# Optimization experiments

Measured on AMD Instinct MI355X. Metric: run time of the kernel, lower is better.

Reference implementation:

```python
import jax, jax.numpy as jnp
import numpy as np

N_HEAD = 12

def setup_inputs() -> dict:
    key = jax.random.key(0)
    ks = jax.random.split(key, 5)
    B, T, C = 2, 2048, 768
    s = 0.02
    return {
        "x": jax.random.normal(ks[0], (B, T, C), jnp.float32),
        "c_attn_w": jax.random.normal(ks[1], (C, 3 * C), jnp.float32) * s,
        "c_attn_b": jax.random.normal(ks[2], (3 * C,), jnp.float32) * s,
        "c_proj_w": jax.random.normal(ks[3], (C, C), jnp.float32) * s,
        "c_proj_b": jax.random.normal(ks[4], (C,), jnp.float32) * s,
    }

def reference(x, c_attn_w, c_attn_b, c_proj_w, c_proj_b):
    B, T, C = x.shape
    H = N_HEAD
    D = C // H
    qkv = x @ c_attn_w + c_attn_b              # [B,T,3C]
    q, k, v = jnp.split(qkv, 3, axis=-1)
    # [B,T,C] -> [B,H,T,D]
    q = q.reshape(B, T, H, D).transpose(0, 2, 1, 3)
    k = k.reshape(B, T, H, D).transpose(0, 2, 1, 3)
    v = v.reshape(B, T, H, D).transpose(0, 2, 1, 3)
    att = jnp.einsum('bhqd,bhkd->bhqk', q, k) * (1.0 / np.sqrt(D))
    causal = jnp.tril(jnp.ones((T, T), bool))  # [T,T]
    att = jnp.where(causal[None, None], att, jnp.float32(-jnp.inf))
    att = jax.nn.softmax(att, axis=-1)
    y = jnp.einsum('bhqk,bhkd->bhqd', att, v)  # [B,H,T,D]
    y = y.transpose(0, 2, 1, 3).reshape(B, T, C)
    return y @ c_proj_w + c_proj_b
```

## Files before the change

kernel.cpp:

```cpp
#include <hip/hip_runtime.h>
#include <hip/hip_bf16.h>


using half4   = __attribute__((ext_vector_type(4))) _Float16;
using half8   = __attribute__((ext_vector_type(8))) _Float16;
using floatx4 = __attribute__((ext_vector_type(4))) float;

#define T_SEQ 2048
#define NHEAD 12
#define HDIM 64
#define C3 2304
#define CDIM 768
#define BT 4096

static __device__ inline _Float16 f2h(float f) { return (_Float16)f; }

__global__ __launch_bounds__(256)
void prologue(const float* __restrict__ x, const float* __restrict__ wa,
              const float* __restrict__ wp, _Float16* __restrict__ xb,
              _Float16* __restrict__ wTa, _Float16* __restrict__ wTp) {
    __shared__ float tile[32][33];
    int blk = blockIdx.x, tid = threadIdx.x;
    if (blk < 2304) {
        const float* w; _Float16* wT; int K, N, bx, by;
        if (blk < 1728) { w = wa; wT = wTa; K = CDIM; N = C3; bx = blk % 72; by = blk / 72; }
        else { int b2 = blk - 1728; w = wp; wT = wTp; K = CDIM; N = CDIM; bx = b2 % 24; by = b2 / 24; }
        int tx = tid & 31, ty = tid >> 5;
        #pragma unroll
        for (int j = 0; j < 32; j += 8) {
            int k = by * 32 + ty + j, n = bx * 32 + tx;
            tile[ty + j][tx] = w[(long)k * N + n];
        }
        __syncthreads();
        #pragma unroll
        for (int j = 0; j < 32; j += 8) {
            int nO = bx * 32 + ty + j, kO = by * 32 + tx;
            wT[(long)nO * K + kO] = f2h(tile[tx][ty + j]);
        }
    } else {
        int b2 = blk - 2304;
        long base = (long)b2 * 1536;
        #pragma unroll
        for (int j = 0; j < 6; ++j) {
            long i = base + j * 256 + tid;
            xb[i] = f2h(x[i]);
        }
    }
}

__global__ __launch_bounds__(256)
void gemm_qkv(const _Float16* __restrict__ A, const _Float16* __restrict__ Bt,
              const float* __restrict__ bias,
              _Float16* __restrict__ Qb, _Float16* __restrict__ Kb,
              _Float16* __restrict__ Vt) {
    __shared__ __align__(16) _Float16 As[128 * 32];
    __shared__ __align__(16) _Float16 Bs[64 * 32];
    const int K = CDIM;
    int tid = threadIdx.x;
    int m0 = blockIdx.x * 128, n0 = blockIdx.y * 64;
    int w = tid >> 6, l = tid & 63;
    int wm = (w >> 1) * 64, wn = (w & 1) * 32;
    int lr = l & 15, lq = l >> 4;

    int ea0 = tid * 8, ea1 = (256 + tid) * 8;
    int ra0 = ea0 >> 5, ca0 = ea0 & 31, ra1 = ea1 >> 5, ca1 = ea1 & 31;
    int eb = tid * 8, rb = eb >> 5, cb = eb & 31;

    floatx4 acc[4][2] = {};

    half8 Ar0 = *(const half8*)&A[(long)(m0 + ra0) * K + ca0];
    half8 Ar1 = *(const half8*)&A[(long)(m0 + ra1) * K + ca1];
    half8 Br  = *(const half8*)&Bt[(long)(n0 + rb) * K + cb];

    for (int kb = 0; kb < K; kb += 32) {
        *(half8*)&As[ea0] = Ar0;
        *(half8*)&As[ea1] = Ar1;
        *(half8*)&Bs[eb]  = Br;
        __syncthreads();
        if (kb + 32 < K) {
            Ar0 = *(const half8*)&A[(long)(m0 + ra0) * K + kb + 32 + ca0];
            Ar1 = *(const half8*)&A[(long)(m0 + ra1) * K + kb + 32 + ca1];
            Br  = *(const half8*)&Bt[(long)(n0 + rb) * K + kb + 32 + cb];
        }
        half8 af[4], bf[2];
        #pragma unroll
        for (int i = 0; i < 4; ++i)
            af[i] = *(const half8*)&As[(wm + i * 16 + lr) * 32 + lq * 8];
        #pragma unroll
        for (int i = 0; i < 2; ++i)
            bf[i] = *(const half8*)&Bs[(wn + i * 16 + lr) * 32 + lq * 8];
        #pragma unroll
        for (int mi = 0; mi < 4; ++mi)
            #pragma unroll
            for (int ni = 0; ni < 2; ++ni)
                acc[mi][ni] = __builtin_amdgcn_mfma_f32_16x16x32_f16(af[mi], bf[ni], acc[mi][ni], 0, 0, 0);
        __syncthreads();
    }

    int region = n0 / CDIM;
    if (region < 2) {
        _Float16* O = region ? Kb : Qb;
        int nc0 = n0 - region * CDIM + wn;
        #pragma unroll
        for (int mi = 0; mi < 4; ++mi)
            #pragma unroll
            for (int ni = 0; ni < 2; ++ni) {
                int col = nc0 + ni * 16 + lr;
                float bsc = bias[region * CDIM + col];
                #pragma unroll
                for (int r = 0; r < 4; ++r) {
                    int row = m0 + wm + mi * 16 + lq * 4 + r;
                    O[(long)row * CDIM + col] = f2h(acc[mi][ni][r] + bsc);
                }
            }
    } else {
        #pragma unroll
        for (int mi = 0; mi < 4; ++mi)
            #pragma unroll
            for (int ni = 0; ni < 2; ++ni) {
                int cv = n0 - 2 * CDIM + wn + ni * 16 + lr;
                float bsc = bias[2 * CDIM + cv];
                int h = cv >> 6, d = cv & 63;
                int t0 = m0 + wm + mi * 16 + lq * 4;
                int bb = t0 >> 11, t = t0 & 2047;
                half4 hv;
                #pragma unroll
                for (int r = 0; r < 4; ++r) hv[r] = f2h(acc[mi][ni][r] + bsc);
                *(half4*)&Vt[(((long)bb * NHEAD + h) * HDIM + d) * T_SEQ + t] = hv;
            }
    }
}

__global__ __launch_bounds__(256)
void gemm_proj(const _Float16* __restrict__ A, const _Float16* __restrict__ Bt,
               const float* __restrict__ bias, float* __restrict__ Cout,
               int M, int N, int K) {
    __shared__ __align__(16) _Float16 As[64 * 32];
    __shared__ __align__(16) _Float16 Bs[64 * 32];
    int tid = threadIdx.x;
    int m0 = blockIdx.x * 64, n0 = blockIdx.y * 64;
    int w = tid >> 6, l = tid & 63;
    int wm = (w >> 1) * 32, wn = (w & 1) * 32;
    int lr = l & 15, lq = l >> 4;

    int e = tid * 8, re = e >> 5, ce = e & 31;

    floatx4 acc[2][2] = {};

    half8 Ar = *(const half8*)&A[(long)(m0 + re) * K + ce];
    half8 Br = *(const half8*)&Bt[(long)(n0 + re) * K + ce];

    for (int kb = 0; kb < K; kb += 32) {
        *(half8*)&As[e] = Ar;
        *(half8*)&Bs[e] = Br;
        __syncthreads();
        if (kb + 32 < K) {
            Ar = *(const half8*)&A[(long)(m0 + re) * K + kb + 32 + ce];
            Br = *(const half8*)&Bt[(long)(n0 + re) * K + kb + 32 + ce];
        }
        half8 af[2], bf[2];
        #pragma unroll
        for (int i = 0; i < 2; ++i) {
            af[i] = *(const half8*)&As[(wm + i * 16 + lr) * 32 + lq * 8];
            bf[i] = *(const half8*)&Bs[(wn + i * 16 + lr) * 32 + lq * 8];
        }
        #pragma unroll
        for (int mi = 0; mi < 2; ++mi)
            #pragma unroll
            for (int ni = 0; ni < 2; ++ni)
                acc[mi][ni] = __builtin_amdgcn_mfma_f32_16x16x32_f16(af[mi], bf[ni], acc[mi][ni], 0, 0, 0);
        __syncthreads();
    }
    #pragma unroll
    for (int mi = 0; mi < 2; ++mi)
        #pragma unroll
        for (int ni = 0; ni < 2; ++ni) {
            int col = n0 + wn + ni * 16 + lr;
            float b = bias[col];
            #pragma unroll
            for (int r = 0; r < 4; ++r) {
                int row = m0 + wm + mi * 16 + lq * 4 + r;
                Cout[(long)row * N + col] = acc[mi][ni][r] + b;
            }
        }
}

__global__ __launch_bounds__(256)
void attn_kernel(const _Float16* __restrict__ Qb, const _Float16* __restrict__ Kb,
                 const _Float16* __restrict__ Vt, _Float16* __restrict__ y) {
    __shared__ __align__(16) _Float16 Ks[64 * 72];
    __shared__ __align__(16) _Float16 Vs[64 * 72];
    __shared__ __align__(16) _Float16 Ps[4][16 * 72];
    int tid = threadIdx.x;
    int w = tid >> 6, l = tid & 63;
    int lr = l & 15, lq = l >> 4;
    int blk = blockIdx.x;
    int bh = blk % (2 * NHEAD);
    int qb = 31 - blk / (2 * NHEAD);
    int b = bh / NHEAD, h = bh % NHEAD;
    int q0 = qb * 64 + w * 16;

    const _Float16* Qp = Qb + (long)b * T_SEQ * CDIM + h * HDIM;
    const _Float16* Kg = Kb + (long)b * T_SEQ * CDIM + h * HDIM;
    const _Float16* Vg = Vt + (long)bh * HDIM * T_SEQ;

    int r0 = tid >> 3, c0 = (tid & 7) * 8;
    int r1 = r0 + 32;

    const float qscale = 0.125f * 1.44269504f;
    half8 aq[2];
    #pragma unroll
    for (int kk = 0; kk < 2; ++kk) {
        aq[kk] = *(const half8*)&Qp[(long)(q0 + lr) * CDIM + kk * 32 + lq * 8];
        #pragma unroll
        for (int j = 0; j < 8; ++j) aq[kk][j] = f2h((float)aq[kk][j] * qscale);
    }

    half8 Kr0 = *(const half8*)&Kg[(long)r0 * CDIM + c0];
    half8 Kr1 = *(const half8*)&Kg[(long)r1 * CDIM + c0];
    half8 Vr0 = *(const half8*)&Vg[(long)r0 * T_SEQ + c0];
    half8 Vr1 = *(const half8*)&Vg[(long)r1 * T_SEQ + c0];

    float psum[4] = {0.f, 0.f, 0.f, 0.f};
    floatx4 acc[4] = {};

    for (int kt = 0; kt <= qb; ++kt) {
        int kbase = kt * 64;
        *(half8*)&Ks[r0 * 72 + c0] = Kr0;
        *(half8*)&Ks[r1 * 72 + c0] = Kr1;
        *(half8*)&Vs[r0 * 72 + c0] = Vr0;
        *(half8*)&Vs[r1 * 72 + c0] = Vr1;
        __syncthreads();
        if (kt < qb) {
            int nb = kbase + 64;
            Kr0 = *(const half8*)&Kg[(long)(nb + r0) * CDIM + c0];
            Kr1 = *(const half8*)&Kg[(long)(nb + r1) * CDIM + c0];
            Vr0 = *(const half8*)&Vg[(long)r0 * T_SEQ + nb + c0];
            Vr1 = *(const half8*)&Vg[(long)r1 * T_SEQ + nb + c0];
        }

        floatx4 sacc[4] = {};
        #pragma unroll
        for (int s = 0; s < 4; ++s)
            #pragma unroll
            for (int kk = 0; kk < 2; ++kk) {
                half8 bk = *(const half8*)&Ks[(s * 16 + lr) * 72 + kk * 32 + lq * 8];
                sacc[s] = __builtin_amdgcn_mfma_f32_16x16x32_f16(aq[kk], bk, sacc[s], 0, 0, 0);
            }

        if (kt == qb) {
            #pragma unroll
            for (int r = 0; r < 4; ++r) {
                int row = q0 + lq * 4 + r;
                #pragma unroll
                for (int s = 0; s < 4; ++s) {
                    float p = (kbase + s * 16 + lr > row) ? 0.f
                              : __builtin_amdgcn_exp2f(sacc[s][r]);
                    psum[r] += p;
                    Ps[w][(lq * 4 + r) * 72 + s * 16 + lr] = f2h(p);
                }
            }
        } else {
            #pragma unroll
            for (int r = 0; r < 4; ++r) {
                #pragma unroll
                for (int s = 0; s < 4; ++s) {
                    float p = __builtin_amdgcn_exp2f(sacc[s][r]);
                    psum[r] += p;
                    Ps[w][(lq * 4 + r) * 72 + s * 16 + lr] = f2h(p);
                }
            }
        }

        half8 ap0 = *(const half8*)&Ps[w][lr * 72 + lq * 8];
        half8 ap1 = *(const half8*)&Ps[w][lr * 72 + 32 + lq * 8];
        #pragma unroll
        for (int n = 0; n < 4; ++n) {
            #pragma unroll
            for (int kk = 0; kk < 2; ++kk) {
                half8 bv = *(const half8*)&Vs[(n * 16 + lr) * 72 + kk * 32 + lq * 8];
                acc[n] = __builtin_amdgcn_mfma_f32_16x16x32_f16(kk ? ap1 : ap0, bv, acc[n], 0, 0, 0);
            }
        }
        __syncthreads();
    }

    float l_i[4];
    #pragma unroll
    for (int r = 0; r < 4; ++r) {
        float s = psum[r];
        #pragma unroll
        for (int off = 1; off < 16; off <<= 1)
            s += __shfl_xor(s, off, 64);
        l_i[r] = s;
    }

    #pragma unroll
    for (int n = 0; n < 4; ++n)
        #pragma unroll
        for (int r = 0; r < 4; ++r) {
            int row = q0 + lq * 4 + r;
            float v = acc[n][r] / l_i[r];
            y[((long)(b * T_SEQ) + row) * CDIM + h * HDIM + n * 16 + lr] = f2h(v);
        }
}

extern "C" void kernel_launch(void* const* d_in, const int* in_sizes, int n_in,
                              void* d_out, int out_size, void* d_ws, size_t ws_size,
                              hipStream_t stream) {
    const float* x      = (const float*)d_in[0];
    const float* w_attn = (const float*)d_in[1];
    const float* b_attn = (const float*)d_in[2];
    const float* w_proj = (const float*)d_in[3];
    const float* b_proj = (const float*)d_in[4];
    float* out = (float*)d_out;

    char* ws = (char*)d_ws;
    _Float16* xb  = (_Float16*)(ws);
    _Float16* wTa = (_Float16*)(ws + 6291456);
    _Float16* wTp = (_Float16*)(ws + 9830400);
    _Float16* Qb  = (_Float16*)(ws + 11010048);
    _Float16* Kb  = (_Float16*)(ws + 17301504);
    _Float16* Vt  = (_Float16*)(ws + 23592960);
    _Float16* yb  = (_Float16*)(ws + 29884416);

    prologue<<<4352, 256, 0, stream>>>(x, w_attn, w_proj, xb, wTa, wTp);

    gemm_qkv<<<dim3(BT / 128, C3 / 64), 256, 0, stream>>>(xb, wTa, b_attn, Qb, Kb, Vt);

    attn_kernel<<<2 * NHEAD * (T_SEQ / 64), 256, 0, stream>>>(Qb, Kb, Vt, yb);

    gemm_proj<<<dim3(BT / 64, CDIM / 64), 256, 0, stream>>>(yb, wTp, b_proj, out, BT, CDIM, CDIM);
}
```

Measured before the change: 157.7 us.

## Split attention over key chunks and merge partials in projection GEMM

The causal attention kernel now splits each query tile's key range into two halves, handled by separate blocks. This doubles the grid and is meant to even out the load imbalance caused by causal masking. Each block writes unnormalised fp32 partial outputs and row sums to workspace. The output projection GEMM now loads both partials, adds them, normalises with a reciprocal and converts to fp16 while staging its A tile. The QKV and projection GEMMs also widen their N tile to 128. The price is extra fp32 global traffic for the partials, larger per-block register and LDS use, and fewer GEMM blocks.

```diff
diff --git a/kernel.cpp b/kernel.cpp
--- a/kernel.cpp
+++ b/kernel.cpp
@@ -12,6 +12,7 @@
 #define C3 2304
 #define CDIM 768
 #define BT 4096
+#define BH 24
 
 static __device__ inline _Float16 f2h(float f) { return (_Float16)f; }
 
@@ -54,45 +55,46 @@
               _Float16* __restrict__ Qb, _Float16* __restrict__ Kb,
               _Float16* __restrict__ Vt) {
     __shared__ __align__(16) _Float16 As[128 * 32];
-    __shared__ __align__(16) _Float16 Bs[64 * 32];
+    __shared__ __align__(16) _Float16 Bs[128 * 32];
     const int K = CDIM;
     int tid = threadIdx.x;
-    int m0 = blockIdx.x * 128, n0 = blockIdx.y * 64;
+    int m0 = blockIdx.x * 128, n0 = blockIdx.y * 128;
     int w = tid >> 6, l = tid & 63;
-    int wm = (w >> 1) * 64, wn = (w & 1) * 32;
+    int wm = (w >> 1) * 64, wn = (w & 1) * 64;
     int lr = l & 15, lq = l >> 4;
 
     int ea0 = tid * 8, ea1 = (256 + tid) * 8;
     int ra0 = ea0 >> 5, ca0 = ea0 & 31, ra1 = ea1 >> 5, ca1 = ea1 & 31;
-    int eb = tid * 8, rb = eb >> 5, cb = eb & 31;
-
-    floatx4 acc[4][2] = {};
+
+    floatx4 acc[4][4] = {};
 
     half8 Ar0 = *(const half8*)&A[(long)(m0 + ra0) * K + ca0];
     half8 Ar1 = *(const half8*)&A[(long)(m0 + ra1) * K + ca1];
-    half8 Br  = *(const half8*)&Bt[(long)(n0 + rb) * K + cb];
+    half8 Br0 = *(const half8*)&Bt[(long)(n0 + ra0) * K + ca0];
+    half8 Br1 = *(const half8*)&Bt[(long)(n0 + ra1) * K + ca1];
 
     for (int kb = 0; kb < K; kb += 32) {
         *(half8*)&As[ea0] = Ar0;
         *(half8*)&As[ea1] = Ar1;
-        *(half8*)&Bs[eb]  = Br;
+        *(half8*)&Bs[ea0] = Br0;
+        *(half8*)&Bs[ea1] = Br1;
         __syncthreads();
         if (kb + 32 < K) {
             Ar0 = *(const half8*)&A[(long)(m0 + ra0) * K + kb + 32 + ca0];
             Ar1 = *(const half8*)&A[(long)(m0 + ra1) * K + kb + 32 + ca1];
-            Br  = *(const half8*)&Bt[(long)(n0 + rb) * K + kb + 32 + cb];
-        }
-        half8 af[4], bf[2];
-        #pragma unroll
-        for (int i = 0; i < 4; ++i)
+            Br0 = *(const half8*)&Bt[(long)(n0 + ra0) * K + kb + 32 + ca0];
+            Br1 = *(const half8*)&Bt[(long)(n0 + ra1) * K + kb + 32 + ca1];
+        }
+        half8 af[4], bf[4];
+        #pragma unroll
+        for (int i = 0; i < 4; ++i) {
             af[i] = *(const half8*)&As[(wm + i * 16 + lr) * 32 + lq * 8];
-        #pragma unroll
-        for (int i = 0; i < 2; ++i)
             bf[i] = *(const half8*)&Bs[(wn + i * 16 + lr) * 32 + lq * 8];
+        }
         #pragma unroll
         for (int mi = 0; mi < 4; ++mi)
             #pragma unroll
-            for (int ni = 0; ni < 2; ++ni)
+            for (int ni = 0; ni < 4; ++ni)
                 acc[mi][ni] = __builtin_amdgcn_mfma_f32_16x16x32_f16(af[mi], bf[ni], acc[mi][ni], 0, 0, 0);
         __syncthreads();
     }
@@ -104,7 +106,7 @@
         #pragma unroll
         for (int mi = 0; mi < 4; ++mi)
             #pragma unroll
-            for (int ni = 0; ni < 2; ++ni) {
+            for (int ni = 0; ni < 4; ++ni) {
                 int col = nc0 + ni * 16 + lr;
                 float bsc = bias[region * CDIM + col];
                 #pragma unroll
@@ -117,7 +119,7 @@
         #pragma unroll
         for (int mi = 0; mi < 4; ++mi)
             #pragma unroll
-            for (int ni = 0; ni < 2; ++ni) {
+            for (int ni = 0; ni < 4; ++ni) {
                 int cv = n0 - 2 * CDIM + wn + ni * 16 + lr;
                 float bsc = bias[2 * CDIM + cv];
                 int h = cv >> 6, d = cv & 63;
@@ -132,62 +134,9 @@
 }
 
 __global__ __launch_bounds__(256)
-void gemm_proj(const _Float16* __restrict__ A, const _Float16* __restrict__ Bt,
-               const float* __restrict__ bias, float* __restrict__ Cout,
-               int M, int N, int K) {
-    __shared__ __align__(16) _Float16 As[64 * 32];
-    __shared__ __align__(16) _Float16 Bs[64 * 32];
-    int tid = threadIdx.x;
-    int m0 = blockIdx.x * 64, n0 = blockIdx.y * 64;
-    int w = tid >> 6, l = tid & 63;
-    int wm = (w >> 1) * 32, wn = (w & 1) * 32;
-    int lr = l & 15, lq = l >> 4;
-
-    int e = tid * 8, re = e >> 5, ce = e & 31;
-
-    floatx4 acc[2][2] = {};
-
-    half8 Ar = *(const half8*)&A[(long)(m0 + re) * K + ce];
-    half8 Br = *(const half8*)&Bt[(long)(n0 + re) * K + ce];
-
-    for (int kb = 0; kb < K; kb += 32) {
-        *(half8*)&As[e] = Ar;
-        *(half8*)&Bs[e] = Br;
-        __syncthreads();
-        if (kb + 32 < K) {
-            Ar = *(const half8*)&A[(long)(m0 + re) * K + kb + 32 + ce];
-            Br = *(const half8*)&Bt[(long)(n0 + re) * K + kb + 32 + ce];
-        }
-        half8 af[2], bf[2];
-        #pragma unroll
-        for (int i = 0; i < 2; ++i) {
-            af[i] = *(const half8*)&As[(wm + i * 16 + lr) * 32 + lq * 8];
-            bf[i] = *(const half8*)&Bs[(wn + i * 16 + lr) * 32 + lq * 8];
-        }
-        #pragma unroll
-        for (int mi = 0; mi < 2; ++mi)
-            #pragma unroll
-            for (int ni = 0; ni < 2; ++ni)
-                acc[mi][ni] = __builtin_amdgcn_mfma_f32_16x16x32_f16(af[mi], bf[ni], acc[mi][ni], 0, 0, 0);
-        __syncthreads();
-    }
-    #pragma unroll
-    for (int mi = 0; mi < 2; ++mi)
-        #pragma unroll
-        for (int ni = 0; ni < 2; ++ni) {
-            int col = n0 + wn + ni * 16 + lr;
-            float b = bias[col];
-            #pragma unroll
-            for (int r = 0; r < 4; ++r) {
-                int row = m0 + wm + mi * 16 + lq * 4 + r;
-                Cout[(long)row * N + col] = acc[mi][ni][r] + b;
-            }
-        }
-}
-
-__global__ __launch_bounds__(256)
 void attn_kernel(const _Float16* __restrict__ Qb, const _Float16* __restrict__ Kb,
-                 const _Float16* __restrict__ Vt, _Float16* __restrict__ y) {
+                 const _Float16* __restrict__ Vt,
+                 float* __restrict__ Pacc, float* __restrict__ Ppsum) {
     __shared__ __align__(16) _Float16 Ks[64 * 72];
     __shared__ __align__(16) _Float16 Vs[64 * 72];
     __shared__ __align__(16) _Float16 Ps[4][16 * 72];
@@ -195,10 +144,15 @@
     int w = tid >> 6, l = tid & 63;
     int lr = l & 15, lq = l >> 4;
     int blk = blockIdx.x;
-    int bh = blk % (2 * NHEAD);
-    int qb = 31 - blk / (2 * NHEAD);
+    int chunk = blk & 1;
+    int rest = blk >> 1;
+    int bh = rest % BH;
+    int qb = 31 - rest / BH;
     int b = bh / NHEAD, h = bh % NHEAD;
     int q0 = qb * 64 + w * 16;
+
+    int lo = chunk ? ((qb + 1) >> 1) : 0;
+    int hi = chunk ? (qb + 1) : ((qb + 1) >> 1);
 
     const _Float16* Qp = Qb + (long)b * T_SEQ * CDIM + h * HDIM;
     const _Float16* Kg = Kb + (long)b * T_SEQ * CDIM + h * HDIM;
@@ -216,22 +170,23 @@
         for (int j = 0; j < 8; ++j) aq[kk][j] = f2h((float)aq[kk][j] * qscale);
     }
 
-    half8 Kr0 = *(const half8*)&Kg[(long)r0 * CDIM + c0];
-    half8 Kr1 = *(const half8*)&Kg[(long)r1 * CDIM + c0];
-    half8 Vr0 = *(const half8*)&Vg[(long)r0 * T_SEQ + c0];
-    half8 Vr1 = *(const half8*)&Vg[(long)r1 * T_SEQ + c0];
+    int kb0 = lo * 64;
+    half8 Kr0 = *(const half8*)&Kg[(long)(kb0 + r0) * CDIM + c0];
+    half8 Kr1 = *(const half8*)&Kg[(long)(kb0 + r1) * CDIM + c0];
+    half8 Vr0 = *(const half8*)&Vg[(long)r0 * T_SEQ + kb0 + c0];
+    half8 Vr1 = *(const half8*)&Vg[(long)r1 * T_SEQ + kb0 + c0];
 
     float psum[4] = {0.f, 0.f, 0.f, 0.f};
     floatx4 acc[4] = {};
 
-    for (int kt = 0; kt <= qb; ++kt) {
+    for (int kt = lo; kt < hi; ++kt) {
         int kbase = kt * 64;
         *(half8*)&Ks[r0 * 72 + c0] = Kr0;
         *(half8*)&Ks[r1 * 72 + c0] = Kr1;
         *(half8*)&Vs[r0 * 72 + c0] = Vr0;
         *(half8*)&Vs[r1 * 72 + c0] = Vr1;
         __syncthreads();
-        if (kt < qb) {
+        if (kt + 1 < hi) {
             int nb = kbase + 64;
             Kr0 = *(const half8*)&Kg[(long)(nb + r0) * CDIM + c0];
             Kr1 = *(const half8*)&Kg[(long)(nb + r1) * CDIM + c0];
@@ -285,23 +240,111 @@
         __syncthreads();
     }
 
-    float l_i[4];
+    float* accb = Pacc + ((long)(chunk * BH + bh) * T_SEQ) * HDIM;
+    float* psb  = Ppsum + (long)(chunk * BH + bh) * T_SEQ;
     #pragma unroll
     for (int r = 0; r < 4; ++r) {
         float s = psum[r];
         #pragma unroll
         for (int off = 1; off < 16; off <<= 1)
             s += __shfl_xor(s, off, 64);
-        l_i[r] = s;
-    }
-
+        if (lr == 0) psb[q0 + lq * 4 + r] = s;
+    }
     #pragma unroll
     for (int n = 0; n < 4; ++n)
         #pragma unroll
-        for (int r = 0; r < 4; ++r) {
-            int row = q0 + lq * 4 + r;
-            float v = acc[n][r] / l_i[r];
-            y[((long)(b * T_SEQ) + row) * CDIM + h * HDIM + n * 16 + lr] = f2h(v);
+        for (int r = 0; r < 4; ++r)
+            accb[(long)(q0 + lq * 4 + r) * HDIM + n * 16 + lr] = acc[n][r];
+}
+
+__global__ __launch_bounds__(256)
+void gemm_proj(const float* __restrict__ Pacc, const float* __restrict__ Ppsum,
+               const _Float16* __restrict__ Bt,
+               const float* __restrict__ bias, float* __restrict__ Cout) {
+    __shared__ __align__(16) _Float16 As[64 * 32];
+    __shared__ __align__(16) _Float16 Bs[128 * 32];
+    const int K = CDIM, N = CDIM;
+    const long CH = (long)BH * T_SEQ * HDIM;
+    int tid = threadIdx.x;
+    int m0 = blockIdx.x * 64, n0 = blockIdx.y * 128;
+    int w = tid >> 6, l = tid & 63;
+    int wm = (w >> 1) * 32, wn = (w & 1) * 64;
+    int lr = l & 15, lq = l >> 4;
+
+    int e = tid * 8, re = e >> 5, ce = e & 31;
+    int eb0 = tid * 8, eb1 = (256 + tid) * 8;
+    int rb0 = eb0 >> 5, cb0 = eb0 & 31, rb1 = eb1 >> 5, cb1 = eb1 & 31;
+
+    int t = m0 + re;
+    int bb = t >> 11, tl = t & 2047;
+    float l0 = Ppsum[((long)bb * NHEAD) * T_SEQ + 0];
+    floatx4 acc[2][4] = {};
+
+    int gc = ce;
+    int hh = gc >> 6, dd = gc & 63;
+    const float* s0 = Pacc + ((long)(bb * NHEAD + hh) * T_SEQ + tl) * HDIM + dd;
+    floatx4 Aa0 = *(const floatx4*)s0;
+    floatx4 Aa1 = *(const floatx4*)(s0 + 4);
+    floatx4 Ab0 = *(const floatx4*)(s0 + CH);
+    floatx4 Ab1 = *(const floatx4*)(s0 + CH + 4);
+    l0 = Ppsum[(long)(bb * NHEAD + hh) * T_SEQ + tl];
+    float l1 = Ppsum[(long)(BH + bb * NHEAD + hh) * T_SEQ + tl];
+
+    half8 Br0 = *(const half8*)&Bt[(long)(n0 + rb0) * K + cb0];
+    half8 Br1 = *(const half8*)&Bt[(long)(n0 + rb1) * K + cb1];
+
+    for (int kb = 0; kb < K; kb += 32) {
+        {
+            float rc = __builtin_amdgcn_rcpf(l0 + l1);
+            half8 h8;
+            #pragma unroll
+            for (int j = 0; j < 4; ++j) {
+                h8[j]     = f2h((Aa0[j] + Ab0[j]) * rc);
+                h8[4 + j] = f2h((Aa1[j] + Ab1[j]) * rc);
+            }
+            *(half8*)&As[e] = h8;
+        }
+        *(half8*)&Bs[eb0] = Br0;
+        *(half8*)&Bs[eb1] = Br1;
+        __syncthreads();
+        if (kb + 32 < K) {
+            gc = kb + 32 + ce;
+            hh = gc >> 6; dd = gc & 63;
+            s0 = Pacc + ((long)(bb * NHEAD + hh) * T_SEQ + tl) * HDIM + dd;
+            Aa0 = *(const floatx4*)s0;
+            Aa1 = *(const floatx4*)(s0 + 4);
+            Ab0 = *(const floatx4*)(s0 + CH);
+            Ab1 = *(const floatx4*)(s0 + CH + 4);
+            l0 = Ppsum[(long)(bb * NHEAD + hh) * T_SEQ + tl];
+            l1 = Ppsum[(long)(BH + bb * NHEAD + hh) * T_SEQ + tl];
+            Br0 = *(const half8*)&Bt[(long)(n0 + rb0) * K + kb + 32 + cb0];
+            Br1 = *(const half8*)&Bt[(long)(n0 + rb1) * K + kb + 32 + cb1];
+        }
+        half8 af[2], bf[4];
+        #pragma unroll
+        for (int i = 0; i < 2; ++i)
+            af[i] = *(const half8*)&As[(wm + i * 16 + lr) * 32 + lq * 8];
+        #pragma unroll
+        for (int i = 0; i < 4; ++i)
+            bf[i] = *(const half8*)&Bs[(wn + i * 16 + lr) * 32 + lq * 8];
+        #pragma unroll
+        for (int mi = 0; mi < 2; ++mi)
+            #pragma unroll
+            for (int ni = 0; ni < 4; ++ni)
+                acc[mi][ni] = __builtin_amdgcn_mfma_f32_16x16x32_f16(af[mi], bf[ni], acc[mi][ni], 0, 0, 0);
+        __syncthreads();
+    }
+    #pragma unroll
+    for (int mi = 0; mi < 2; ++mi)
+        #pragma unroll
+        for (int ni = 0; ni < 4; ++ni) {
+            int col = n0 + wn + ni * 16 + lr;
+            float b = bias[col];
+            #pragma unroll
+            for (int r = 0; r < 4; ++r) {
+                int row = m0 + wm + mi * 16 + lq * 4 + r;
+                Cout[(long)row * N + col] = acc[mi][ni][r] + b;
+            }
         }
 }
 
@@ -316,19 +359,20 @@
     float* out = (float*)d_out;
 
     char* ws = (char*)d_ws;
-    _Float16* xb  = (_Float16*)(ws);
-    _Float16* wTa = (_Float16*)(ws + 6291456);
-    _Float16* wTp = (_Float16*)(ws + 9830400);
-    _Float16* Qb  = (_Float16*)(ws + 11010048);
-    _Float16* Kb  = (_Float16*)(ws + 17301504);
-    _Float16* Vt  = (_Float16*)(ws + 23592960);
-    _Float16* yb  = (_Float16*)(ws + 29884416);
+    _Float16* xb   = (_Float16*)(ws);
+    _Float16* wTa  = (_Float16*)(ws + 6291456);
+    _Float16* wTp  = (_Float16*)(ws + 9830400);
+    _Float16* Qb   = (_Float16*)(ws + 11010048);
+    _Float16* Kb   = (_Float16*)(ws + 17301504);
+    _Float16* Vt   = (_Float16*)(ws + 23592960);
+    float*    Pacc = (float*)(ws + 29884416);
+    float*    Ppsum= (float*)(ws + 55050240);
 
     prologue<<<4352, 256, 0, stream>>>(x, w_attn, w_proj, xb, wTa, wTp);
 
-    gemm_qkv<<<dim3(BT / 128, C3 / 64), 256, 0, stream>>>(xb, wTa, b_attn, Qb, Kb, Vt);
-
-    attn_kernel<<<2 * NHEAD * (T_SEQ / 64), 256, 0, stream>>>(Qb, Kb, Vt, yb);
-
-    gemm_proj<<<dim3(BT / 64, CDIM / 64), 256, 0, stream>>>(yb, wTp, b_proj, out, BT, CDIM, CDIM);
-}
+    gemm_qkv<<<dim3(BT / 128, C3 / 128), 256, 0, stream>>>(xb, wTa, b_attn, Qb, Kb, Vt);
+
+    attn_kernel<<<2 * BH * (T_SEQ / 64), 256, 0, stream>>>(Qb, Kb, Vt, Pacc, Ppsum);
+
+    gemm_proj<<<dim3(BT / 64, CDIM / 128), 256, 0, stream>>>(Pacc, Ppsum, wTp, b_proj, out);
+}
```

After: 163.1 us. 3.4% more time.

## Double K-step depth in GEMMs and widen attention key tiles to 128

Applied to the files above, without the earlier changes.

Both GEMMs now stage 64-wide K slices in padded shared memory (stride 72), which halves the number of barrier-synchronised iterations. The projection GEMM also switches to 64x128 output tiles. The attention kernel processes 128 keys per iteration instead of 64, with a 128-wide V/P tile, so it syncs half as often. In exchange it raises register and LDS use, and it does extra masked work on the diagonal block when qb is even.

```diff
diff --git a/kernel.cpp b/kernel.cpp
--- a/kernel.cpp
+++ b/kernel.cpp
@@ -12,6 +12,7 @@
 #define C3 2304
 #define CDIM 768
 #define BT 4096
+#define BH 24
 
 static __device__ inline _Float16 f2h(float f) { return (_Float16)f; }
 
@@ -53,8 +54,8 @@
               const float* __restrict__ bias,
               _Float16* __restrict__ Qb, _Float16* __restrict__ Kb,
               _Float16* __restrict__ Vt) {
-    __shared__ __align__(16) _Float16 As[128 * 32];
-    __shared__ __align__(16) _Float16 Bs[64 * 32];
+    __shared__ __align__(16) _Float16 As[128 * 72];
+    __shared__ __align__(16) _Float16 Bs[64 * 72];
     const int K = CDIM;
     int tid = threadIdx.x;
     int m0 = blockIdx.x * 128, n0 = blockIdx.y * 64;
@@ -62,38 +63,49 @@
     int wm = (w >> 1) * 64, wn = (w & 1) * 32;
     int lr = l & 15, lq = l >> 4;
 
-    int ea0 = tid * 8, ea1 = (256 + tid) * 8;
-    int ra0 = ea0 >> 5, ca0 = ea0 & 31, ra1 = ea1 >> 5, ca1 = ea1 & 31;
-    int eb = tid * 8, rb = eb >> 5, cb = eb & 31;
+    int rs = tid >> 3, cs = (tid & 7) * 8;
 
     floatx4 acc[4][2] = {};
 
-    half8 Ar0 = *(const half8*)&A[(long)(m0 + ra0) * K + ca0];
-    half8 Ar1 = *(const half8*)&A[(long)(m0 + ra1) * K + ca1];
-    half8 Br  = *(const half8*)&Bt[(long)(n0 + rb) * K + cb];
-
-    for (int kb = 0; kb < K; kb += 32) {
-        *(half8*)&As[ea0] = Ar0;
-        *(half8*)&As[ea1] = Ar1;
-        *(half8*)&Bs[eb]  = Br;
-        __syncthreads();
-        if (kb + 32 < K) {
-            Ar0 = *(const half8*)&A[(long)(m0 + ra0) * K + kb + 32 + ca0];
-            Ar1 = *(const half8*)&A[(long)(m0 + ra1) * K + kb + 32 + ca1];
-            Br  = *(const half8*)&Bt[(long)(n0 + rb) * K + kb + 32 + cb];
-        }
-        half8 af[4], bf[2];
-        #pragma unroll
-        for (int i = 0; i < 4; ++i)
-            af[i] = *(const half8*)&As[(wm + i * 16 + lr) * 32 + lq * 8];
-        #pragma unroll
-        for (int i = 0; i < 2; ++i)
-            bf[i] = *(const half8*)&Bs[(wn + i * 16 + lr) * 32 + lq * 8];
-        #pragma unroll
-        for (int mi = 0; mi < 4; ++mi)
-            #pragma unroll
-            for (int ni = 0; ni < 2; ++ni)
-                acc[mi][ni] = __builtin_amdgcn_mfma_f32_16x16x32_f16(af[mi], bf[ni], acc[mi][ni], 0, 0, 0);
+    half8 Ar[4], Br[2];
+    #pragma unroll
+    for (int j = 0; j < 4; ++j)
+        Ar[j] = *(const half8*)&A[(long)(m0 + j * 32 + rs) * K + cs];
+    #pragma unroll
+    for (int j = 0; j < 2; ++j)
+        Br[j] = *(const half8*)&Bt[(long)(n0 + j * 32 + rs) * K + cs];
+
+    for (int kb = 0; kb < K; kb += 64) {
+        #pragma unroll
+        for (int j = 0; j < 4; ++j)
+            *(half8*)&As[(j * 32 + rs) * 72 + cs] = Ar[j];
+        #pragma unroll
+        for (int j = 0; j < 2; ++j)
+            *(half8*)&Bs[(j * 32 + rs) * 72 + cs] = Br[j];
+        __syncthreads();
+        if (kb + 64 < K) {
+            #pragma unroll
+            for (int j = 0; j < 4; ++j)
+                Ar[j] = *(const half8*)&A[(long)(m0 + j * 32 + rs) * K + kb + 64 + cs];
+            #pragma unroll
+            for (int j = 0; j < 2; ++j)
+                Br[j] = *(const half8*)&Bt[(long)(n0 + j * 32 + rs) * K + kb + 64 + cs];
+        }
+        #pragma unroll
+        for (int kh = 0; kh < 2; ++kh) {
+            half8 af[4], bf[2];
+            #pragma unroll
+            for (int i = 0; i < 4; ++i)
+                af[i] = *(const half8*)&As[(wm + i * 16 + lr) * 72 + kh * 32 + lq * 8];
+            #pragma unroll
+            for (int i = 0; i < 2; ++i)
+                bf[i] = *(const half8*)&Bs[(wn + i * 16 + lr) * 72 + kh * 32 + lq * 8];
+            #pragma unroll
+            for (int mi = 0; mi < 4; ++mi)
+                #pragma unroll
+                for (int ni = 0; ni < 2; ++ni)
+                    acc[mi][ni] = __builtin_amdgcn_mfma_f32_16x16x32_f16(af[mi], bf[ni], acc[mi][ni], 0, 0, 0);
+        }
         __syncthreads();
     }
 
@@ -133,48 +145,65 @@
 
 __global__ __launch_bounds__(256)
 void gemm_proj(const _Float16* __restrict__ A, const _Float16* __restrict__ Bt,
-               const float* __restrict__ bias, float* __restrict__ Cout,
-               int M, int N, int K) {
-    __shared__ __align__(16) _Float16 As[64 * 32];
-    __shared__ __align__(16) _Float16 Bs[64 * 32];
+               const float* __restrict__ bias, float* __restrict__ Cout) {
+    __shared__ __align__(16) _Float16 As[64 * 72];
+    __shared__ __align__(16) _Float16 Bs[128 * 72];
+    const int K = CDIM, N = CDIM;
     int tid = threadIdx.x;
-    int m0 = blockIdx.x * 64, n0 = blockIdx.y * 64;
+    int m0 = blockIdx.x * 64, n0 = blockIdx.y * 128;
     int w = tid >> 6, l = tid & 63;
-    int wm = (w >> 1) * 32, wn = (w & 1) * 32;
+    int wm = (w >> 1) * 32, wn = (w & 1) * 64;
     int lr = l & 15, lq = l >> 4;
 
-    int e = tid * 8, re = e >> 5, ce = e & 31;
-
-    floatx4 acc[2][2] = {};
-
-    half8 Ar = *(const half8*)&A[(long)(m0 + re) * K + ce];
-    half8 Br = *(const half8*)&Bt[(long)(n0 + re) * K + ce];
-
-    for (int kb = 0; kb < K; kb += 32) {
-        *(half8*)&As[e] = Ar;
-        *(half8*)&Bs[e] = Br;
-        __syncthreads();
-        if (kb + 32 < K) {
-            Ar = *(const half8*)&A[(long)(m0 + re) * K + kb + 32 + ce];
-            Br = *(const half8*)&Bt[(long)(n0 + re) * K + kb + 32 + ce];
-        }
-        half8 af[2], bf[2];
-        #pragma unroll
-        for (int i = 0; i < 2; ++i) {
-            af[i] = *(const half8*)&As[(wm + i * 16 + lr) * 32 + lq * 8];
-            bf[i] = *(const half8*)&Bs[(wn + i * 16 + lr) * 32 + lq * 8];
-        }
-        #pragma unroll
-        for (int mi = 0; mi < 2; ++mi)
-            #pragma unroll
-            for (int ni = 0; ni < 2; ++ni)
-                acc[mi][ni] = __builtin_amdgcn_mfma_f32_16x16x32_f16(af[mi], bf[ni], acc[mi][ni], 0, 0, 0);
+    int rs = tid >> 3, cs = (tid & 7) * 8;
+
+    floatx4 acc[2][4] = {};
+
+    half8 Ar[2], Br[4];
+    #pragma unroll
+    for (int j = 0; j < 2; ++j)
+        Ar[j] = *(const half8*)&A[(long)(m0 + j * 32 + rs) * K + cs];
+    #pragma unroll
+    for (int j = 0; j < 4; ++j)
+        Br[j] = *(const half8*)&Bt[(long)(n0 + j * 32 + rs) * K + cs];
+
+    for (int kb = 0; kb < K; kb += 64) {
+        #pragma unroll
+        for (int j = 0; j < 2; ++j)
+            *(half8*)&As[(j * 32 + rs) * 72 + cs] = Ar[j];
+        #pragma unroll
+        for (int j = 0; j < 4; ++j)
+            *(half8*)&Bs[(j * 32 + rs) * 72 + cs] = Br[j];
+        __syncthreads();
+        if (kb + 64 < K) {
+            #pragma unroll
+            for (int j = 0; j < 2; ++j)
+                Ar[j] = *(const half8*)&A[(long)(m0 + j * 32 + rs) * K + kb + 64 + cs];
+            #pragma unroll
+            for (int j = 0; j < 4; ++j)
+                Br[j] = *(const half8*)&Bt[(long)(n0 + j * 32 + rs) * K + kb + 64 + cs];
+        }
+        #pragma unroll
+        for (int kh = 0; kh < 2; ++kh) {
+            half8 af[2], bf[4];
+            #pragma unroll
+            for (int i = 0; i < 2; ++i)
+                af[i] = *(const half8*)&As[(wm + i * 16 + lr) * 72 + kh * 32 + lq * 8];
+            #pragma unroll
+            for (int i = 0; i < 4; ++i)
+                bf[i] = *(const half8*)&Bs[(wn + i * 16 + lr) * 72 + kh * 32 + lq * 8];
+            #pragma unroll
+            for (int mi = 0; mi < 2; ++mi)
+                #pragma unroll
+                for (int ni = 0; ni < 4; ++ni)
+                    acc[mi][ni] = __builtin_amdgcn_mfma_f32_16x16x32_f16(af[mi], bf[ni], acc[mi][ni], 0, 0, 0);
+        }
         __syncthreads();
     }
     #pragma unroll
     for (int mi = 0; mi < 2; ++mi)
         #pragma unroll
-        for (int ni = 0; ni < 2; ++ni) {
+        for (int ni = 0; ni < 4; ++ni) {
             int col = n0 + wn + ni * 16 + lr;
             float b = bias[col];
             #pragma unroll
@@ -188,15 +217,15 @@
 __global__ __launch_bounds__(256)
 void attn_kernel(const _Float16* __restrict__ Qb, const _Float16* __restrict__ Kb,
                  const _Float16* __restrict__ Vt, _Float16* __restrict__ y) {
-    __shared__ __align__(16) _Float16 Ks[64 * 72];
-    __shared__ __align__(16) _Float16 Vs[64 * 72];
-    __shared__ __align__(16) _Float16 Ps[4][16 * 72];
+    __shared__ __align__(16) _Float16 Ks[128 * 72];
+    __shared__ __align__(16) _Float16 Vs[64 * 136];
+    __shared__ __align__(16) _Float16 Ps[4][16 * 136];
     int tid = threadIdx.x;
     int w = tid >> 6, l = tid & 63;
     int lr = l & 15, lq = l >> 4;
     int blk = blockIdx.x;
-    int bh = blk % (2 * NHEAD);
-    int qb = 31 - blk / (2 * NHEAD);
+    int bh = blk % BH;
+    int qb = 31 - blk / BH;
     int b = bh / NHEAD, h = bh % NHEAD;
     int q0 = qb * 64 + w * 16;
 
@@ -204,8 +233,8 @@
     const _Float16* Kg = Kb + (long)b * T_SEQ * CDIM + h * HDIM;
     const _Float16* Vg = Vt + (long)bh * HDIM * T_SEQ;
 
-    int r0 = tid >> 3, c0 = (tid & 7) * 8;
-    int r1 = r0 + 32;
+    int kr = tid >> 3, kc = (tid & 7) * 8;
+    int vr = tid >> 4, vc = (tid & 15) * 8;
 
     const float qscale = 0.125f * 1.44269504f;
     half8 aq[2];
@@ -216,70 +245,80 @@
         for (int j = 0; j < 8; ++j) aq[kk][j] = f2h((float)aq[kk][j] * qscale);
     }
 
-    half8 Kr0 = *(const half8*)&Kg[(long)r0 * CDIM + c0];
-    half8 Kr1 = *(const half8*)&Kg[(long)r1 * CDIM + c0];
-    half8 Vr0 = *(const half8*)&Vg[(long)r0 * T_SEQ + c0];
-    half8 Vr1 = *(const half8*)&Vg[(long)r1 * T_SEQ + c0];
+    int nk = (qb + 2) >> 1;
+
+    half8 Kr[4], Vr[4];
+    #pragma unroll
+    for (int j = 0; j < 4; ++j) {
+        Kr[j] = *(const half8*)&Kg[(long)(j * 32 + kr) * CDIM + kc];
+        Vr[j] = *(const half8*)&Vg[(long)(j * 16 + vr) * T_SEQ + vc];
+    }
 
     float psum[4] = {0.f, 0.f, 0.f, 0.f};
     floatx4 acc[4] = {};
 
-    for (int kt = 0; kt <= qb; ++kt) {
-        int kbase = kt * 64;
-        *(half8*)&Ks[r0 * 72 + c0] = Kr0;
-        *(half8*)&Ks[r1 * 72 + c0] = Kr1;
-        *(half8*)&Vs[r0 * 72 + c0] = Vr0;
-        *(half8*)&Vs[r1 * 72 + c0] = Vr1;
-        __syncthreads();
-        if (kt < qb) {
-            int nb = kbase + 64;
-            Kr0 = *(const half8*)&Kg[(long)(nb + r0) * CDIM + c0];
-            Kr1 = *(const half8*)&Kg[(long)(nb + r1) * CDIM + c0];
-            Vr0 = *(const half8*)&Vg[(long)r0 * T_SEQ + nb + c0];
-            Vr1 = *(const half8*)&Vg[(long)r1 * T_SEQ + nb + c0];
-        }
-
-        floatx4 sacc[4] = {};
-        #pragma unroll
-        for (int s = 0; s < 4; ++s)
-            #pragma unroll
-            for (int kk = 0; kk < 2; ++kk) {
-                half8 bk = *(const half8*)&Ks[(s * 16 + lr) * 72 + kk * 32 + lq * 8];
-                sacc[s] = __builtin_amdgcn_mfma_f32_16x16x32_f16(aq[kk], bk, sacc[s], 0, 0, 0);
-            }
-
-        if (kt == qb) {
+    for (int kt = 0; kt < nk; ++kt) {
+        int kbase = kt * 128;
+        #pragma unroll
+        for (int j = 0; j < 4; ++j) {
+            *(half8*)&Ks[(j * 32 + kr) * 72 + kc] = Kr[j];
+            *(half8*)&Vs[(j * 16 + vr) * 136 + vc] = Vr[j];
+        }
+        __syncthreads();
+        if (kt + 1 < nk) {
+            int nb = kbase + 128;
+            #pragma unroll
+            for (int j = 0; j < 4; ++j) {
+                Kr[j] = *(const half8*)&Kg[(long)(nb + j * 32 + kr) * CDIM + kc];
+                Vr[j] = *(const half8*)&Vg[(long)(j * 16 + vr) * T_SEQ + nb + vc];
+            }
+        }
+
+        floatx4 sacc[8];
+        #pragma unroll
+        for (int s = 0; s < 8; ++s) sacc[s] = floatx4{0.f, 0.f, 0.f, 0.f};
+        #pragma unroll
+        for (int s = 0; s < 8; ++s)
+            #pragma unroll
+            for (int kh = 0; kh < 2; ++kh) {
+                half8 bk = *(const half8*)&Ks[(s * 16 + lr) * 72 + kh * 32 + lq * 8];
+                sacc[s] = __builtin_amdgcn_mfma_f32_16x16x32_f16(aq[kh], bk, sacc[s], 0, 0, 0);
+            }
+
+        if (kt == nk - 1) {
             #pragma unroll
             for (int r = 0; r < 4; ++r) {
                 int row = q0 + lq * 4 + r;
                 #pragma unroll
-                for (int s = 0; s < 4; ++s) {
+                for (int s = 0; s < 8; ++s) {
                     float p = (kbase + s * 16 + lr > row) ? 0.f
                               : __builtin_amdgcn_exp2f(sacc[s][r]);
                     psum[r] += p;
-                    Ps[w][(lq * 4 + r) * 72 + s * 16 + lr] = f2h(p);
+                    Ps[w][(lq * 4 + r) * 136 + s * 16 + lr] = f2h(p);
                 }
             }
         } else {
             #pragma unroll
             for (int r = 0; r < 4; ++r) {
                 #pragma unroll
-                for (int s = 0; s < 4; ++s) {
+                for (int s = 0; s < 8; ++s) {
                     float p = __builtin_amdgcn_exp2f(sacc[s][r]);
                     psum[r] += p;
-                    Ps[w][(lq * 4 + r) * 72 + s * 16 + lr] = f2h(p);
+                    Ps[w][(lq * 4 + r) * 136 + s * 16 + lr] = f2h(p);
                 }
             }
         }
 
-        half8 ap0 = *(const half8*)&Ps[w][lr * 72 + lq * 8];
-        half8 ap1 = *(const half8*)&Ps[w][lr * 72 + 32 + lq * 8];
+        half8 ap[4];
+        #pragma unroll
+        for (int kk = 0; kk < 4; ++kk)
+            ap[kk] = *(const half8*)&Ps[w][lr * 136 + kk * 32 + lq * 8];
         #pragma unroll
         for (int n = 0; n < 4; ++n) {
             #pragma unroll
-            for (int kk = 0; kk < 2; ++kk) {
-                half8 bv = *(const half8*)&Vs[(n * 16 + lr) * 72 + kk * 32 + lq * 8];
-                acc[n] = __builtin_amdgcn_mfma_f32_16x16x32_f16(kk ? ap1 : ap0, bv, acc[n], 0, 0, 0);
+            for (int kk = 0; kk < 4; ++kk) {
+                half8 bv = *(const half8*)&Vs[(n * 16 + lr) * 136 + kk * 32 + lq * 8];
+                acc[n] = __builtin_amdgcn_mfma_f32_16x16x32_f16(ap[kk], bv, acc[n], 0, 0, 0);
             }
         }
         __syncthreads();
@@ -328,7 +367,7 @@
 
     gemm_qkv<<<dim3(BT / 128, C3 / 64), 256, 0, stream>>>(xb, wTa, b_attn, Qb, Kb, Vt);
 
-    attn_kernel<<<2 * NHEAD * (T_SEQ / 64), 256, 0, stream>>>(Qb, Kb, Vt, yb);
-
-    gemm_proj<<<dim3(BT / 64, CDIM / 64), 256, 0, stream>>>(yb, wTp, b_proj, out, BT, CDIM, CDIM);
-}
+    attn_kernel<<<BH * (T_SEQ / 64), 256, 0, stream>>>(Qb, Kb, Vt, yb);
+
+    gemm_proj<<<dim3(BT / 64, CDIM / 128), 256, 0, stream>>>(yb, wTp, b_proj, out);
+}
```

Measured after the change: 152.6 us. 3.2% less time.
